# Optimization experiments

Hardware: AMD Instinct MI355X
Metric: run time of the kernel (lower is better)

Reference implementation:

```python
import jax, jax.numpy as jnp
import numpy as np

# Dims: M=batch, T=time frames, B=bottleneck channels, H=intermediate channels, KK=kernel size
M, T, B, H, KK = 8, 4000, 128, 512, 3
DILATION = 2
EPS = 1e-8  # gLN eps (ConvTasNet convention)


def prelu(x, a):
    return jnp.where(x >= 0, x, a * x)


def gln(x, gamma, beta):
    # global layer norm over (time, channel) per sample; x: [M, T, C]
    m = jnp.mean(x, axis=(1, 2), keepdims=True)
    v = jnp.mean((x - m) ** 2, axis=(1, 2), keepdims=True)
    return gamma * (x - m) / jnp.sqrt(v + EPS) + beta


def depthwise_conv_same_reflect(x, w):
    # x: [M, C, L], w: [C, K]; dilation 1, 'same' padding with reflect mode
    K = w.shape[1]
    pl = (K - 1) // 2
    xp = jnp.pad(x, ((0, 0), (0, 0), (pl, K - 1 - pl)), mode='reflect')
    return jax.lax.conv_general_dilated(
        xp, w[:, None, :], (1,), 'VALID',
        feature_group_count=x.shape[1], dimension_numbers=('NCH', 'OIH', 'NCH'))


def setup_inputs() -> dict:
    key = jax.random.key(0)
    ks = jax.random.split(key, 12)
    f32 = jnp.float32
    return {
        'x': jax.random.normal(ks[0], (M, T, B), f32),
        'conv1_w': jax.random.normal(ks[1], (H, B), f32) * 0.05,
        'prelu1_a': jnp.asarray(0.25, f32),
        'norm1_g': jnp.ones((H,), f32),
        'norm1_b': jnp.zeros((H,), f32),
        'off_dw_w': jax.random.normal(ks[2], (H, KK), f32) * 0.02,
        'odc_prelu_a': jnp.asarray(0.25, f32),
        'off_pw_w': jax.random.normal(ks[3], (KK, H), f32) * 0.02,
        'opc_prelu_a': jnp.asarray(0.25, f32),
        'dw_w': jax.random.normal(ks[4], (H, KK), f32) * 0.05,
        'dw_b': jax.random.normal(ks[5], (H,), f32) * 0.01,
        'prelu2_a': jnp.asarray(0.25, f32),
        'norm2_g': jnp.ones((H,), f32),
        'norm2_b': jnp.zeros((H,), f32),
        'pw_w': jax.random.normal(ks[6], (B, H), f32) * 0.05,
    }


def reference(x, conv1_w, prelu1_a, norm1_g, norm1_b,
              off_dw_w, odc_prelu_a, off_pw_w, opc_prelu_a,
              dw_w, dw_b, prelu2_a, norm2_g, norm2_b, pw_w):
    dtype = x.dtype
    residual = x
    # 1x1 bottleneck conv -> PReLU -> gLN
    h = jnp.einsum('mtb,hb->mth', x, conv1_w)
    h = gln(prelu(h, prelu1_a), norm1_g, norm1_b)
    hc = jnp.moveaxis(h, 1, 2)  # [M, H, T]

    # --- offset prediction branch (PackedDeformConv1d) ---
    off = depthwise_conv_same_reflect(hc, off_dw_w)          # [M, H, T]
    off = prelu(off, odc_prelu_a)
    off = jnp.einsum('mct,kc->mkt', off, off_pw_w)           # [M, KK, T]
    off = prelu(off, opc_prelu_a)
    offsets = jnp.moveaxis(off, 1, 2)                        # [M, T, KK]

    # --- deformable depthwise conv (same padding, reflect) ---
    pad_tot = DILATION * (KK - 1)
    pl = pad_tot // 2
    xp = jnp.pad(hc, ((0, 0), (0, 0), (pl, pad_tot - pl)), mode='reflect')  # [M,H,Lp]
    Lp = T + pad_tot
    dil_pos = (jnp.arange(KK) * DILATION).astype(dtype)      # [KK]: 0, d, 2d
    t0 = jnp.arange(T, dtype=dtype)[:, None]                 # [T,1]
    Tpos = t0 + dil_pos[None, :] + offsets                   # [M,T,KK]
    Tpos = jnp.clip(Tpos, t0, t0 + dil_pos[-1])              # constrain to receptive field
    U = jnp.clip(jnp.floor(Tpos).astype(jnp.int32), 0, Lp - 2)
    Uf = U.astype(dtype)
    g0 = jax.nn.relu(1.0 - jnp.abs(Uf - Tpos))               # [M,T,KK]
    g1 = jax.nn.relu(1.0 - jnp.abs(Uf + 1.0 - Tpos))
    idx = jnp.broadcast_to(U.reshape(M, 1, T * KK), (M, H, T * KK))
    s0 = jnp.take_along_axis(xp, idx, axis=2).reshape(M, H, T, KK)
    s1 = jnp.take_along_axis(xp, idx + 1, axis=2).reshape(M, H, T, KK)
    sampled = g0[:, None] * s0 + g1[:, None] * s1            # [M,H,T,KK]
    y = jnp.einsum('mhtk,hk->mht', sampled, dw_w) + dw_b[None, :, None]

    # PReLU -> gLN -> 1x1 conv back to B channels, residual add
    y = jnp.moveaxis(y, 1, 2)                                # [M,T,H]
    y = gln(prelu(y, prelu2_a), norm2_g, norm2_b)
    out = jnp.einsum('mth,bh->mtb', y, pw_w)
    return out + residual
```

## Files before the change

kernel.cpp:

```cpp
#include <hip/hip_runtime.h>

#define Mdim 8
#define Tdim 4000
#define Bdim 128
#define Hdim 512
#define NPER (Tdim*Hdim)
#define EPSG 1e-8f

typedef __attribute__((ext_vector_type(8))) short short8;
typedef __attribute__((ext_vector_type(4))) float floatx4;

static __device__ __forceinline__ float bits2f(unsigned short s) {
  union { unsigned int u; float f; } v; v.u = ((unsigned int)s) << 16; return v.f;
}
static __device__ __forceinline__ unsigned short f2bits(float f) {
  union { float f; unsigned int u; } v; v.f = f;
  unsigned int u = v.u;
  u += 0x7fffu + ((u >> 16) & 1u);
  return (unsigned short)(u >> 16);
}
static __device__ __forceinline__ short8 pack8(const float4& a, const float4& b) {
  short8 v;
  v[0]=(short)f2bits(a.x); v[1]=(short)f2bits(a.y); v[2]=(short)f2bits(a.z); v[3]=(short)f2bits(a.w);
  v[4]=(short)f2bits(b.x); v[5]=(short)f2bits(b.y); v[6]=(short)f2bits(b.z); v[7]=(short)f2bits(b.w);
  return v;
}

__global__ __launch_bounds__(256) void k_conv1(
    const float* __restrict__ x,
    const float* __restrict__ w1,
    const float* __restrict__ a1p,
    unsigned short* __restrict__ Hbuf,
    float2* __restrict__ part1)
{
  __shared__ __align__(16) unsigned short ldsW[64*136];
  __shared__ __align__(16) unsigned short ltile[64*72];
  __shared__ float red[512];

  const int tid = threadIdx.x;
  const int t0 = blockIdx.x * 64;
  const int m  = blockIdx.y;

  const int lane = tid & 63, wv = tid >> 6, quad = lane >> 4, l16 = lane & 15;
  int tr = t0 + wv*16 + l16;
  int trc = tr < Tdim ? tr : Tdim-1;
  const float* xrow = x + ((size_t)m*Tdim + trc)*Bdim;
  short8 afr[4];
  #pragma unroll
  for (int ks = 0; ks < 4; ++ks) {
    float4 fa = *(const float4*)&xrow[ks*32 + quad*8];
    float4 fb = *(const float4*)&xrow[ks*32 + quad*8 + 4];
    afr[ks] = pack8(fa, fb);
  }

  const float a1 = a1p[0];
  float lsum = 0.f, lss = 0.f;

  for (int hc = 0; hc < 8; ++hc) {
    const int h0 = hc * 64;
    __syncthreads();
    #pragma unroll
    for (int it = 0; it < 4; ++it) {
      int idx = (it*256 + tid) * 8;
      int r = idx >> 7, c = idx & 127;
      float4 fa = *(const float4*)&w1[(size_t)(h0 + r)*Bdim + c];
      float4 fb = *(const float4*)&w1[(size_t)(h0 + r)*Bdim + c + 4];
      *(short8*)&ldsW[r*136 + c] = pack8(fa, fb);
    }
    __syncthreads();

    floatx4 acc[4] = {};
    #pragma unroll
    for (int ks = 0; ks < 4; ++ks) {
      #pragma unroll
      for (int nt = 0; nt < 4; ++nt) {
        short8 bfr = *(const short8*)&ldsW[(nt*16 + l16)*136 + ks*32 + quad*8];
        acc[nt] = __builtin_amdgcn_mfma_f32_16x16x32_bf16(afr[ks], bfr, acc[nt], 0, 0, 0);
      }
    }

    #pragma unroll
    for (int nt = 0; nt < 4; ++nt) {
      int hl = nt*16 + l16;
      #pragma unroll
      for (int r = 0; r < 4; ++r) {
        int tl = wv*16 + quad*4 + r;
        float v = acc[nt][r];
        v = v >= 0.f ? v : a1 * v;
        if (t0 + tl < Tdim) { lsum += v; lss += v*v; }
        ltile[tl*72 + hl] = f2bits(v);
      }
    }
    __syncthreads();
    {
      int tr2 = tid >> 2, ck = (tid & 3) * 16;
      int tg = t0 + tr2;
      if (tg < Tdim) {
        unsigned short* dst = &Hbuf[((size_t)m*Tdim + tg)*Hdim + h0 + ck];
        *(short8*)&dst[0] = *(const short8*)&ltile[tr2*72 + ck];
        *(short8*)&dst[8] = *(const short8*)&ltile[tr2*72 + ck + 8];
      }
    }
  }

  red[tid] = lsum; red[256 + tid] = lss;
  __syncthreads();
  for (int s = 128; s > 0; s >>= 1) {
    if (tid < s) { red[tid] += red[tid + s]; red[256+tid] += red[256+tid+s]; }
    __syncthreads();
  }
  if (tid == 0)
    part1[(size_t)m*63 + blockIdx.x] = make_float2(red[0], red[256]);
}

__global__ __launch_bounds__(256) void k_deform(
    const unsigned short* __restrict__ Hbuf,
    const float2* __restrict__ part1,
    const float* __restrict__ g1w,
    const float* __restrict__ b1w,
    const float* __restrict__ odw,
    const float* __restrict__ aodcp,
    const float* __restrict__ opw,
    const float* __restrict__ aopcp,
    const float* __restrict__ dww,
    const float* __restrict__ dwb,
    const float* __restrict__ a2p,
    unsigned short* __restrict__ Ybuf,
    float2* __restrict__ part2)
{
  __shared__ float s_stats[2];
  __shared__ float rsum[4], rss[4];
  const int tid = threadIdx.x, lane = tid & 63, w = tid >> 6;
  const int t = blockIdx.x*4 + w;
  const int m = blockIdx.y;

  if (tid < 64) {
    float2 p = (lane < 63) ? part1[(size_t)m*63 + lane] : make_float2(0.f, 0.f);
    float s = p.x, q = p.y;
    #pragma unroll
    for (int st = 32; st > 0; st >>= 1) { s += __shfl_xor(s, st); q += __shfl_xor(q, st); }
    if (lane == 0) { s_stats[0] = s; s_stats[1] = q; }
  }
  __syncthreads();
  const float invn = 1.0f/(float)NPER;
  const float mean1 = s_stats[0]*invn;
  const float var1  = fmaxf(s_stats[1]*invn - mean1*mean1, 0.f);
  const float inv1  = 1.0f/sqrtf(var1 + EPSG);

  const int c8 = lane*8;
  const unsigned short* base = Hbuf + (size_t)m*Tdim*Hdim;

  float g1v[8], b1v[8];
  #pragma unroll
  for (int j = 0; j < 8; j += 4) {
    *(float4*)&g1v[j] = *(const float4*)&g1w[c8 + j];
    *(float4*)&b1v[j] = *(const float4*)&b1w[c8 + j];
  }

  float o0 = 0.f, o1 = 0.f, o2 = 0.f;
  {
    const float aodc = aodcp[0];
    float wod[24], q0v[8], q1v[8], q2v[8];
    #pragma unroll
    for (int j = 0; j < 8; j += 4) {
      *(float4*)&q0v[j] = *(const float4*)&opw[c8 + j];
      *(float4*)&q1v[j] = *(const float4*)&opw[Hdim + c8 + j];
      *(float4*)&q2v[j] = *(const float4*)&opw[2*Hdim + c8 + j];
    }
    #pragma unroll
    for (int j = 0; j < 24; j += 4)
      *(float4*)&wod[j] = *(const float4*)&odw[c8*3 + j];

    const int tm1 = (t == 0) ? 1 : t-1;
    const int tp1 = (t == Tdim-1) ? Tdim-2 : t+1;
    short8 hm = *(const short8*)&base[(size_t)tm1*Hdim + c8];
    short8 hz = *(const short8*)&base[(size_t)t  *Hdim + c8];
    short8 hp = *(const short8*)&base[(size_t)tp1*Hdim + c8];

    #pragma unroll
    for (int j = 0; j < 8; ++j) {
      float A = g1v[j] * inv1;
      float C = b1v[j] - mean1*A;
      float fm = fmaf(A, bits2f((unsigned short)hm[j]), C);
      float fz = fmaf(A, bits2f((unsigned short)hz[j]), C);
      float fp = fmaf(A, bits2f((unsigned short)hp[j]), C);
      float d = fm*wod[j*3+0] + fz*wod[j*3+1] + fp*wod[j*3+2];
      d = d >= 0.f ? d : aodc*d;
      o0 = fmaf(d, q0v[j], o0);
      o1 = fmaf(d, q1v[j], o1);
      o2 = fmaf(d, q2v[j], o2);
    }
    #pragma unroll
    for (int s = 32; s > 0; s >>= 1) {
      o0 += __shfl_xor(o0, s);
      o1 += __shfl_xor(o1, s);
      o2 += __shfl_xor(o2, s);
    }
  }

  const float aopc = aopcp[0];
  const float a2   = a2p[0];
  int I0[3], I1[3]; float G0[3], G1[3], GS[3];
  {
    const float tf = (float)t;
    float offs[3] = {o0, o1, o2};
    #pragma unroll
    for (int k = 0; k < 3; ++k) {
      float off = offs[k];
      off = off >= 0.f ? off : aopc*off;
      float pos = tf + (float)(2*k) + off;
      pos = fminf(fmaxf(pos, tf), tf + 4.0f);
      int U = (int)floorf(pos);
      if (U > Tdim + 2) U = Tdim + 2;
      float Uf = (float)U;
      G0[k] = fmaxf(0.f, 1.f - fabsf(Uf - pos));
      G1[k] = fmaxf(0.f, 1.f - fabsf(Uf + 1.f - pos));
      GS[k] = G0[k] + G1[k];
      int ia = U - 2; ia = ia < 0 ? -ia : ia; if (ia > Tdim-1) ia = 2*(Tdim-1) - ia;
      int ib = U - 1; ib = ib < 0 ? -ib : ib; if (ib > Tdim-1) ib = 2*(Tdim-1) - ib;
      I0[k] = ia; I1[k] = ib;
    }
  }

  short8 s0v[3], s1v[3];
  #pragma unroll
  for (int k = 0; k < 3; ++k) {
    s0v[k] = *(const short8*)&base[(size_t)I0[k]*Hdim + c8];
    s1v[k] = *(const short8*)&base[(size_t)I1[k]*Hdim + c8];
  }

  float bv[8], wd[24];
  #pragma unroll
  for (int j = 0; j < 8; j += 4)
    *(float4*)&bv[j] = *(const float4*)&dwb[c8 + j];
  #pragma unroll
  for (int j = 0; j < 24; j += 4)
    *(float4*)&wd[j] = *(const float4*)&dww[c8*3 + j];

  float lsum = 0.f, lss = 0.f;
  short8 yv;
  #pragma unroll
  for (int j = 0; j < 8; ++j) {
    float A = g1v[j] * inv1;
    float C = b1v[j] - mean1*A;
    float w0 = wd[j*3+0], w1 = wd[j*3+1], w2 = wd[j*3+2];
    float ybase = fmaf(C, w0*GS[0] + w1*GS[1] + w2*GS[2], bv[j]);
    float t0s = fmaf(G1[0], bits2f((unsigned short)s1v[0][j]), G0[0]*bits2f((unsigned short)s0v[0][j]));
    float t1s = fmaf(G1[1], bits2f((unsigned short)s1v[1][j]), G0[1]*bits2f((unsigned short)s0v[1][j]));
    float t2s = fmaf(G1[2], bits2f((unsigned short)s1v[2][j]), G0[2]*bits2f((unsigned short)s0v[2][j]));
    float acc = w0*t0s + w1*t1s + w2*t2s;
    float y = fmaf(A, acc, ybase);
    float p = y >= 0.f ? y : a2*y;
    lsum += p; lss += p*p;
    yv[j] = (short)f2bits(p);
  }
  *(short8*)&Ybuf[((size_t)m*Tdim + t)*Hdim + c8] = yv;

  #pragma unroll
  for (int s = 32; s > 0; s >>= 1) {
    lsum += __shfl_xor(lsum, s);
    lss  += __shfl_xor(lss, s);
  }
  if (lane == 0) { rsum[w] = lsum; rss[w] = lss; }
  __syncthreads();
  if (tid == 0)
    part2[(size_t)m*1000 + blockIdx.x] =
      make_float2(rsum[0]+rsum[1]+rsum[2]+rsum[3], rss[0]+rss[1]+rss[2]+rss[3]);
}

__global__ __launch_bounds__(64) void k_w2(
    const float2* __restrict__ part2,
    const float* __restrict__ g2w,
    const float* __restrict__ b2w,
    const float* __restrict__ pww,
    unsigned short* __restrict__ W2,
    float* __restrict__ const2)
{
  const int bid = blockIdx.x;
  const int m = bid >> 7, b = bid & 127;
  const int tid = threadIdx.x;

  float s = 0.f, q = 0.f;
  for (int i = tid; i < 1000; i += 64) {
    float2 p = part2[(size_t)m*1000 + i];
    s += p.x; q += p.y;
  }
  #pragma unroll
  for (int st = 32; st > 0; st >>= 1) { s += __shfl_xor(s, st); q += __shfl_xor(q, st); }

  const float invn = 1.0f/(float)NPER;
  const float mean2 = s*invn;
  const float var2  = fmaxf(q*invn - mean2*mean2, 0.f);
  const float inv2  = 1.0f/sqrtf(var2 + EPSG);

  const int j8 = tid*8;
  float g2v[8], b2v[8], pv[8];
  #pragma unroll
  for (int j = 0; j < 8; j += 4) {
    *(float4*)&g2v[j] = *(const float4*)&g2w[j8 + j];
    *(float4*)&b2v[j] = *(const float4*)&b2w[j8 + j];
    *(float4*)&pv[j]  = *(const float4*)&pww[(size_t)b*Hdim + j8 + j];
  }
  float csum = 0.f;
  short8 wv8;
  #pragma unroll
  for (int j = 0; j < 8; ++j) {
    float A = g2v[j] * inv2;
    float C = b2v[j] - mean2*A;
    csum = fmaf(C, pv[j], csum);
    wv8[j] = (short)f2bits(A*pv[j]);
  }
  *(short8*)&W2[((size_t)m*Bdim + b)*Hdim + j8] = wv8;

  #pragma unroll
  for (int st = 32; st > 0; st >>= 1) csum += __shfl_down(csum, st);
  if (tid == 0) const2[m*Bdim + b] = csum;
}

__global__ __launch_bounds__(256) void k_out(
    const unsigned short* __restrict__ Ybuf,
    const unsigned short* __restrict__ W2,
    const float* __restrict__ const2,
    const float* __restrict__ x,
    float* __restrict__ out)
{
  __shared__ __align__(16) unsigned short ldsW[64*136];
  __shared__ __align__(16) float ltf[64*68];
  const int tid = threadIdx.x;
  const int t0 = blockIdx.x*64;
  const int n0 = blockIdx.y*64;
  const int m  = blockIdx.z;
  const int lane = tid & 63, wv = tid >> 6, quad = lane >> 4, l16 = lane & 15;
  int tr = t0 + wv*16 + l16;
  int trc = tr < Tdim ? tr : Tdim-1;
  const unsigned short* arow = Ybuf + ((size_t)m*Tdim + trc)*Hdim;
  floatx4 acc[4] = {};
  for (int kc = 0; kc < 4; ++kc) {
    __syncthreads();
    #pragma unroll
    for (int it = 0; it < 4; ++it) {
      int idx = (it*256 + tid)*8;
      int r = idx >> 7, c = idx & 127;
      *(short8*)&ldsW[r*136 + c] =
        *(const short8*)&W2[((size_t)m*Bdim + n0 + r)*Hdim + kc*128 + c];
    }
    __syncthreads();
    #pragma unroll
    for (int ks = 0; ks < 4; ++ks) {
      short8 afr = *(const short8*)&arow[kc*128 + ks*32 + quad*8];
      #pragma unroll
      for (int nt = 0; nt < 4; ++nt) {
        short8 bfr = *(const short8*)&ldsW[(nt*16 + l16)*136 + ks*32 + quad*8];
        acc[nt] = __builtin_amdgcn_mfma_f32_16x16x32_bf16(afr, bfr, acc[nt], 0, 0, 0);
      }
    }
  }
  __syncthreads();
  #pragma unroll
  for (int nt = 0; nt < 4; ++nt) {
    int bl = nt*16 + l16;
    float cb = const2[m*Bdim + n0 + bl];
    #pragma unroll
    for (int r = 0; r < 4; ++r) {
      int tl = wv*16 + quad*4 + r;
      ltf[tl*68 + bl] = acc[nt][r] + cb;
    }
  }
  __syncthreads();
  {
    int tr2 = tid >> 2, ck = (tid & 3) * 16;
    int tg = t0 + tr2;
    if (tg < Tdim) {
      const float* xr = &x[((size_t)m*Tdim + tg)*Bdim + n0 + ck];
      float* orow = &out[((size_t)m*Tdim + tg)*Bdim + n0 + ck];
      #pragma unroll
      for (int j = 0; j < 4; ++j) {
        float4 v = *(const float4*)&ltf[tr2*68 + ck + j*4];
        float4 rx = *(const float4*)&xr[j*4];
        v.x += rx.x; v.y += rx.y; v.z += rx.z; v.w += rx.w;
        *(float4*)&orow[j*4] = v;
      }
    }
  }
}

extern "C" void kernel_launch(void* const* d_in, const int* in_sizes, int n_in,
                              void* d_out, int out_size, void* d_ws, size_t ws_size,
                              hipStream_t stream)
{
  (void)in_sizes; (void)n_in; (void)out_size; (void)ws_size;
  const float* x    = (const float*)d_in[0];
  const float* w1   = (const float*)d_in[1];
  const float* a1   = (const float*)d_in[2];
  const float* g1   = (const float*)d_in[3];
  const float* b1   = (const float*)d_in[4];
  const float* odw  = (const float*)d_in[5];
  const float* aodc = (const float*)d_in[6];
  const float* opw  = (const float*)d_in[7];
  const float* aopc = (const float*)d_in[8];
  const float* dww  = (const float*)d_in[9];
  const float* dwb  = (const float*)d_in[10];
  const float* a2   = (const float*)d_in[11];
  const float* g2   = (const float*)d_in[12];
  const float* b2   = (const float*)d_in[13];
  const float* pww  = (const float*)d_in[14];
  float* out = (float*)d_out;

  char* ws = (char*)d_ws;
  const size_t OFF_P1 = 0;
  const size_t OFF_C2 = 4096;
  const size_t OFF_P2 = 8192;
  const size_t OFF_W2 = 72192;
  const size_t OFF_H  = 1120768;
  const size_t OFF_Y  = 33888768;
  float2* part1  = (float2*)(ws + OFF_P1);
  float*  const2 = (float*)(ws + OFF_C2);
  float2* part2  = (float2*)(ws + OFF_P2);
  unsigned short* W2   = (unsigned short*)(ws + OFF_W2);
  unsigned short* Hbuf = (unsigned short*)(ws + OFF_H);
  unsigned short* Ybuf = (unsigned short*)(ws + OFF_Y);

  k_conv1 <<<dim3(63, 8), 256, 0, stream>>>(x, w1, a1, Hbuf, part1);
  k_deform<<<dim3(1000, 8), 256, 0, stream>>>(Hbuf, part1, g1, b1, odw, aodc, opw, aopc, dww, dwb, a2, Ybuf, part2);
  k_w2    <<<dim3(1024), 64, 0, stream>>>(part2, g2, b2, pww, W2, const2);
  k_out   <<<dim3(63, 2, 8), 256, 0, stream>>>(Ybuf, W2, const2, x, out);
}
```

Measured before the change: 178.5 us.

## Split conv1 over H halves and process two timesteps per deform wave

k_conv1's grid gains a second dimension that splits the H channel loop into two halves, doubling the block count from 504 to 1008 so more of the GPU is occupied. k_deform now handles two time steps per wavefront, loading the neighbouring Hbuf rows and per-channel weights once for both and hoisting those loads ahead of the stats barrier. Partial-sum layouts and workspace offsets change to match. The cost is more registers per thread in k_deform, and each conv1 block now repeats its x-fragment load for half the work.

```diff
diff --git a/kernel.cpp b/kernel.cpp
--- a/kernel.cpp
+++ b/kernel.cpp
@@ -39,7 +39,8 @@
 
   const int tid = threadIdx.x;
   const int t0 = blockIdx.x * 64;
-  const int m  = blockIdx.y;
+  const int hh = blockIdx.y;
+  const int m  = blockIdx.z;
 
   const int lane = tid & 63, wv = tid >> 6, quad = lane >> 4, l16 = lane & 15;
   int tr = t0 + wv*16 + l16;
@@ -56,8 +57,8 @@
   const float a1 = a1p[0];
   float lsum = 0.f, lss = 0.f;
 
-  for (int hc = 0; hc < 8; ++hc) {
-    const int h0 = hc * 64;
+  for (int hc = 0; hc < 4; ++hc) {
+    const int h0 = (hh*4 + hc) * 64;
     __syncthreads();
     #pragma unroll
     for (int it = 0; it < 4; ++it) {
@@ -110,7 +111,7 @@
     __syncthreads();
   }
   if (tid == 0)
-    part1[(size_t)m*63 + blockIdx.x] = make_float2(red[0], red[256]);
+    part1[((size_t)m*2 + hh)*63 + blockIdx.x] = make_float2(red[0], red[256]);
 }
 
 __global__ __launch_bounds__(256) void k_deform(
@@ -131,12 +132,34 @@
   __shared__ float s_stats[2];
   __shared__ float rsum[4], rss[4];
   const int tid = threadIdx.x, lane = tid & 63, w = tid >> 6;
-  const int t = blockIdx.x*4 + w;
+  const int tb = blockIdx.x*8 + w*2;
   const int m = blockIdx.y;
+  const int c8 = lane*8;
+  const unsigned short* base = Hbuf + (size_t)m*Tdim*Hdim;
+
+  short8 hrow[2][3];
+  #pragma unroll
+  for (int tt = 0; tt < 2; ++tt) {
+    int t = tb + tt;
+    int tm1 = (t == 0) ? 1 : t-1;
+    int tp1 = (t == Tdim-1) ? Tdim-2 : t+1;
+    hrow[tt][0] = *(const short8*)&base[(size_t)tm1*Hdim + c8];
+    hrow[tt][1] = *(const short8*)&base[(size_t)t  *Hdim + c8];
+    hrow[tt][2] = *(const short8*)&base[(size_t)tp1*Hdim + c8];
+  }
+  float g1v[8], b1v[8];
+  #pragma unroll
+  for (int j = 0; j < 8; j += 4) {
+    *(float4*)&g1v[j] = *(const float4*)&g1w[c8 + j];
+    *(float4*)&b1v[j] = *(const float4*)&b1w[c8 + j];
+  }
 
   if (tid < 64) {
-    float2 p = (lane < 63) ? part1[(size_t)m*63 + lane] : make_float2(0.f, 0.f);
-    float s = p.x, q = p.y;
+    float s = 0.f, q = 0.f;
+    for (int i = lane; i < 126; i += 64) {
+      float2 p = part1[(size_t)m*126 + i];
+      s += p.x; q += p.y;
+    }
     #pragma unroll
     for (int st = 32; st > 0; st >>= 1) { s += __shfl_xor(s, st); q += __shfl_xor(q, st); }
     if (lane == 0) { s_stats[0] = s; s_stats[1] = q; }
@@ -147,17 +170,7 @@
   const float var1  = fmaxf(s_stats[1]*invn - mean1*mean1, 0.f);
   const float inv1  = 1.0f/sqrtf(var1 + EPSG);
 
-  const int c8 = lane*8;
-  const unsigned short* base = Hbuf + (size_t)m*Tdim*Hdim;
-
-  float g1v[8], b1v[8];
-  #pragma unroll
-  for (int j = 0; j < 8; j += 4) {
-    *(float4*)&g1v[j] = *(const float4*)&g1w[c8 + j];
-    *(float4*)&b1v[j] = *(const float4*)&b1w[c8 + j];
-  }
-
-  float o0 = 0.f, o1 = 0.f, o2 = 0.f;
+  float oa[2][3] = {};
   {
     const float aodc = aodcp[0];
     float wod[24], q0v[8], q1v[8], q2v[8];
@@ -171,63 +184,65 @@
     for (int j = 0; j < 24; j += 4)
       *(float4*)&wod[j] = *(const float4*)&odw[c8*3 + j];
 
-    const int tm1 = (t == 0) ? 1 : t-1;
-    const int tp1 = (t == Tdim-1) ? Tdim-2 : t+1;
-    short8 hm = *(const short8*)&base[(size_t)tm1*Hdim + c8];
-    short8 hz = *(const short8*)&base[(size_t)t  *Hdim + c8];
-    short8 hp = *(const short8*)&base[(size_t)tp1*Hdim + c8];
-
     #pragma unroll
     for (int j = 0; j < 8; ++j) {
       float A = g1v[j] * inv1;
       float C = b1v[j] - mean1*A;
-      float fm = fmaf(A, bits2f((unsigned short)hm[j]), C);
-      float fz = fmaf(A, bits2f((unsigned short)hz[j]), C);
-      float fp = fmaf(A, bits2f((unsigned short)hp[j]), C);
-      float d = fm*wod[j*3+0] + fz*wod[j*3+1] + fp*wod[j*3+2];
-      d = d >= 0.f ? d : aodc*d;
-      o0 = fmaf(d, q0v[j], o0);
-      o1 = fmaf(d, q1v[j], o1);
-      o2 = fmaf(d, q2v[j], o2);
+      #pragma unroll
+      for (int tt = 0; tt < 2; ++tt) {
+        float fm = fmaf(A, bits2f((unsigned short)hrow[tt][0][j]), C);
+        float fz = fmaf(A, bits2f((unsigned short)hrow[tt][1][j]), C);
+        float fp = fmaf(A, bits2f((unsigned short)hrow[tt][2][j]), C);
+        float d = fm*wod[j*3+0] + fz*wod[j*3+1] + fp*wod[j*3+2];
+        d = d >= 0.f ? d : aodc*d;
+        oa[tt][0] = fmaf(d, q0v[j], oa[tt][0]);
+        oa[tt][1] = fmaf(d, q1v[j], oa[tt][1]);
+        oa[tt][2] = fmaf(d, q2v[j], oa[tt][2]);
+      }
     }
     #pragma unroll
     for (int s = 32; s > 0; s >>= 1) {
-      o0 += __shfl_xor(o0, s);
-      o1 += __shfl_xor(o1, s);
-      o2 += __shfl_xor(o2, s);
+      #pragma unroll
+      for (int tt = 0; tt < 2; ++tt) {
+        oa[tt][0] += __shfl_xor(oa[tt][0], s);
+        oa[tt][1] += __shfl_xor(oa[tt][1], s);
+        oa[tt][2] += __shfl_xor(oa[tt][2], s);
+      }
     }
   }
 
   const float aopc = aopcp[0];
   const float a2   = a2p[0];
-  int I0[3], I1[3]; float G0[3], G1[3], GS[3];
-  {
-    const float tf = (float)t;
-    float offs[3] = {o0, o1, o2};
+  int I0[2][3], I1[2][3]; float G0[2][3], G1[2][3], GS[2][3];
+  #pragma unroll
+  for (int tt = 0; tt < 2; ++tt) {
+    const float tf = (float)(tb + tt);
     #pragma unroll
     for (int k = 0; k < 3; ++k) {
-      float off = offs[k];
+      float off = oa[tt][k];
       off = off >= 0.f ? off : aopc*off;
       float pos = tf + (float)(2*k) + off;
       pos = fminf(fmaxf(pos, tf), tf + 4.0f);
       int U = (int)floorf(pos);
       if (U > Tdim + 2) U = Tdim + 2;
       float Uf = (float)U;
-      G0[k] = fmaxf(0.f, 1.f - fabsf(Uf - pos));
-      G1[k] = fmaxf(0.f, 1.f - fabsf(Uf + 1.f - pos));
-      GS[k] = G0[k] + G1[k];
+      G0[tt][k] = fmaxf(0.f, 1.f - fabsf(Uf - pos));
+      G1[tt][k] = fmaxf(0.f, 1.f - fabsf(Uf + 1.f - pos));
+      GS[tt][k] = G0[tt][k] + G1[tt][k];
       int ia = U - 2; ia = ia < 0 ? -ia : ia; if (ia > Tdim-1) ia = 2*(Tdim-1) - ia;
       int ib = U - 1; ib = ib < 0 ? -ib : ib; if (ib > Tdim-1) ib = 2*(Tdim-1) - ib;
-      I0[k] = ia; I1[k] = ib;
-    }
-  }
-
-  short8 s0v[3], s1v[3];
-  #pragma unroll
-  for (int k = 0; k < 3; ++k) {
-    s0v[k] = *(const short8*)&base[(size_t)I0[k]*Hdim + c8];
-    s1v[k] = *(const short8*)&base[(size_t)I1[k]*Hdim + c8];
-  }
+      I0[tt][k] = ia; I1[tt][k] = ib;
+    }
+  }
+
+  short8 s0v[2][3], s1v[2][3];
+  #pragma unroll
+  for (int tt = 0; tt < 2; ++tt)
+    #pragma unroll
+    for (int k = 0; k < 3; ++k) {
+      s0v[tt][k] = *(const short8*)&base[(size_t)I0[tt][k]*Hdim + c8];
+      s1v[tt][k] = *(const short8*)&base[(size_t)I1[tt][k]*Hdim + c8];
+    }
 
   float bv[8], wd[24];
   #pragma unroll
@@ -238,23 +253,28 @@
     *(float4*)&wd[j] = *(const float4*)&dww[c8*3 + j];
 
   float lsum = 0.f, lss = 0.f;
-  short8 yv;
+  short8 yv[2];
   #pragma unroll
   for (int j = 0; j < 8; ++j) {
     float A = g1v[j] * inv1;
     float C = b1v[j] - mean1*A;
     float w0 = wd[j*3+0], w1 = wd[j*3+1], w2 = wd[j*3+2];
-    float ybase = fmaf(C, w0*GS[0] + w1*GS[1] + w2*GS[2], bv[j]);
-    float t0s = fmaf(G1[0], bits2f((unsigned short)s1v[0][j]), G0[0]*bits2f((unsigned short)s0v[0][j]));
-    float t1s = fmaf(G1[1], bits2f((unsigned short)s1v[1][j]), G0[1]*bits2f((unsigned short)s0v[1][j]));
-    float t2s = fmaf(G1[2], bits2f((unsigned short)s1v[2][j]), G0[2]*bits2f((unsigned short)s0v[2][j]));
-    float acc = w0*t0s + w1*t1s + w2*t2s;
-    float y = fmaf(A, acc, ybase);
-    float p = y >= 0.f ? y : a2*y;
-    lsum += p; lss += p*p;
-    yv[j] = (short)f2bits(p);
-  }
-  *(short8*)&Ybuf[((size_t)m*Tdim + t)*Hdim + c8] = yv;
+    #pragma unroll
+    for (int tt = 0; tt < 2; ++tt) {
+      float ybase = fmaf(C, w0*GS[tt][0] + w1*GS[tt][1] + w2*GS[tt][2], bv[j]);
+      float t0s = fmaf(G1[tt][0], bits2f((unsigned short)s1v[tt][0][j]), G0[tt][0]*bits2f((unsigned short)s0v[tt][0][j]));
+      float t1s = fmaf(G1[tt][1], bits2f((unsigned short)s1v[tt][1][j]), G0[tt][1]*bits2f((unsigned short)s0v[tt][1][j]));
+      float t2s = fmaf(G1[tt][2], bits2f((unsigned short)s1v[tt][2][j]), G0[tt][2]*bits2f((unsigned short)s0v[tt][2][j]));
+      float acc = w0*t0s + w1*t1s + w2*t2s;
+      float y = fmaf(A, acc, ybase);
+      float p = y >= 0.f ? y : a2*y;
+      lsum += p; lss += p*p;
+      yv[tt][j] = (short)f2bits(p);
+    }
+  }
+  #pragma unroll
+  for (int tt = 0; tt < 2; ++tt)
+    *(short8*)&Ybuf[((size_t)m*Tdim + tb + tt)*Hdim + c8] = yv[tt];
 
   #pragma unroll
   for (int s = 32; s > 0; s >>= 1) {
@@ -264,7 +284,7 @@
   if (lane == 0) { rsum[w] = lsum; rss[w] = lss; }
   __syncthreads();
   if (tid == 0)
-    part2[(size_t)m*1000 + blockIdx.x] =
+    part2[(size_t)m*500 + blockIdx.x] =
       make_float2(rsum[0]+rsum[1]+rsum[2]+rsum[3], rss[0]+rss[1]+rss[2]+rss[3]);
 }
 
@@ -281,8 +301,8 @@
   const int tid = threadIdx.x;
 
   float s = 0.f, q = 0.f;
-  for (int i = tid; i < 1000; i += 64) {
-    float2 p = part2[(size_t)m*1000 + i];
+  for (int i = tid; i < 500; i += 64) {
+    float2 p = part2[(size_t)m*500 + i];
     s += p.x; q += p.y;
   }
   #pragma unroll
@@ -408,11 +428,11 @@
 
   char* ws = (char*)d_ws;
   const size_t OFF_P1 = 0;
-  const size_t OFF_C2 = 4096;
-  const size_t OFF_P2 = 8192;
-  const size_t OFF_W2 = 72192;
-  const size_t OFF_H  = 1120768;
-  const size_t OFF_Y  = 33888768;
+  const size_t OFF_C2 = 8192;
+  const size_t OFF_P2 = 12288;
+  const size_t OFF_W2 = 44288;
+  const size_t OFF_H  = 1092864;
+  const size_t OFF_Y  = 33860864;
   float2* part1  = (float2*)(ws + OFF_P1);
   float*  const2 = (float*)(ws + OFF_C2);
   float2* part2  = (float2*)(ws + OFF_P2);
@@ -420,8 +440,8 @@
   unsigned short* Hbuf = (unsigned short*)(ws + OFF_H);
   unsigned short* Ybuf = (unsigned short*)(ws + OFF_Y);
 
-  k_conv1 <<<dim3(63, 8), 256, 0, stream>>>(x, w1, a1, Hbuf, part1);
-  k_deform<<<dim3(1000, 8), 256, 0, stream>>>(Hbuf, part1, g1, b1, odw, aodc, opw, aopc, dww, dwb, a2, Ybuf, part2);
+  k_conv1 <<<dim3(63, 2, 8), 256, 0, stream>>>(x, w1, a1, Hbuf, part1);
+  k_deform<<<dim3(500, 8), 256, 0, stream>>>(Hbuf, part1, g1, b1, odw, aodc, opw, aopc, dww, dwb, a2, Ybuf, part2);
   k_w2    <<<dim3(1024), 64, 0, stream>>>(part2, g2, b2, pww, W2, const2);
   k_out   <<<dim3(63, 2, 8), 256, 0, stream>>>(Ybuf, W2, const2, x, out);
 }
```

Result: faster. 164.1 us (-8.1%).
